# Optimization experiments

Measured on AMD Instinct MI355X. Metric: run time of the kernel, lower is better.

## Reference

```python
import jax, jax.numpy as jnp
import numpy as np

B, T, E, K, NNEG = 128, 512, 128, 4, 64


def setup_inputs() -> dict:
    key = jax.random.key(0)
    k1, k2, k3, k4 = jax.random.split(key, 4)
    base_payload = jax.random.normal(k1, (B, T, E), dtype=jnp.float32)
    mapped_ctx_payload = jax.random.normal(k2, (B, T, E, K), dtype=jnp.float32)
    seq_lens = jax.random.randint(k3, (B,), 1, T + 1, dtype=jnp.int32)
    # valid positions mask over the flattened (B*T) pool of possible negatives
    valid = (jnp.arange(T)[None, :] < seq_lens[:, None]).reshape(-1)  # [B*T]
    logits = jnp.where(valid, 0.0, -1e30)[None, :]                    # [1, B*T]
    logits = jnp.broadcast_to(logits, (B, B * T))
    # mirrors torch.multinomial(mask, n_negatives): one draw set per batch row
    sample_ids = jax.random.categorical(k4, logits, shape=(NNEG, B)).T.astype(jnp.int32)
    return {
        "base_payload": base_payload,
        "mapped_ctx_payload": mapped_ctx_payload,
        "seq_lens": seq_lens,
        "sample_ids": sample_ids,
    }


def reference(base_payload, mapped_ctx_payload, seq_lens, sample_ids):
    b, t, e = base_payload.shape
    n_steps = mapped_ctx_payload.shape[-1]
    # length mask [b, t]
    len_mask = (jnp.arange(t)[None, :] < seq_lens[:, None]).astype(base_payload.dtype)
    # zero context embeddings past each sequence's length
    trimmed_mce = mapped_ctx_payload * len_mask[:, :, None, None]  # [b, t, e, n_steps]
    # gather sampled negatives from the flattened base embedding pool
    neg_samples = base_payload.reshape(b * t, e)[sample_ids]  # [b, n_neg, e]

    step_losses = []
    for i in range(1, n_steps + 1):
        ce_i = trimmed_mce[:, : t - i, :, i - 1]   # [b, t-i, e]
        be_i = base_payload[:, i:]                  # [b, t-i, e]
        positive_pred = jnp.sum(ce_i * be_i, axis=-1)             # [b, t-i]
        neg_pred = jnp.einsum('bse,bne->bsn', ce_i, neg_samples)  # [b, t-i, n_neg]
        logits = jnp.concatenate([positive_pred[..., None], neg_pred], axis=-1)
        step_losses.append(-jax.nn.log_softmax(logits, axis=-1)[:, :, 0].mean())
    return jnp.stack(step_losses).mean()
```

## Files before the change

kernel.cpp:

```cpp
#include <hip/hip_runtime.h>
#include <math.h>

#define NB 128
#define NT 512
#define NEDIM 128
#define NNEG 64
#define SCHUNK 32
#define NBLK (NB * (NT / SCHUNK))

typedef __bf16 bf16x8 __attribute__((ext_vector_type(8)));
typedef float  f32x4  __attribute__((ext_vector_type(4)));

__launch_bounds__(256, 3)
__global__ void cpc_mfma_kernel(const float* __restrict__ base,
                                const float* __restrict__ mce,
                                const int*  __restrict__ seq_lens,
                                const int*  __restrict__ sample_ids,
                                float* __restrict__ ws)
{
    const int b    = blockIdx.y;
    const int s0   = blockIdx.x * SCHUNK;
    const int slot = b * (NT / SCHUNK) + blockIdx.x;
    const int L    = seq_lens[b];
    const float LOG65 = 4.1743873f;
    const float wgt[4] = {1.f/261632.f, 1.f/261120.f, 1.f/260608.f, 1.f/260096.f};

    if (s0 >= L) {
        if (threadIdx.x == 0) {
            float c = 0.f;
            #pragma unroll
            for (int i = 1; i <= 4; ++i) {
                int hi = min(SCHUNK, (NT - i) - s0);
                if (hi > 0) c += (float)hi * LOG65 * wgt[i - 1];
            }
            ws[slot] = c;
        }
        return;
    }

    __shared__ __bf16 Afrag[2048 * 8];
    __shared__ __bf16 Bfrag[1024 * 8];
    __shared__ float  pos_lds[128];
    __shared__ float  wsum[4];

    const int tid  = threadIdx.x;
    const int lane = tid & 63;
    const int w    = tid >> 6;
    const int q    = lane >> 4;
    const int fl   = lane & 15;

    const float4* mce4 = (const float4*)mce;

    #pragma unroll
    for (int it = 0; it < 2; ++it) {
        int g  = tid + 256 * it;
        int s  = g & 31;
        int eb = g >> 5;
        const float4* src = mce4 + (size_t)(b * NT + s0 + s) * NEDIM + eb * 8;
        float4 v[8];
        #pragma unroll
        for (int u = 0; u < 8; ++u) v[u] = src[u];
        const float* vf = (const float*)v;
        int Cs = (eb >> 2) * 8 + (s >> 2);
        int base_chunk = Cs * 64 + (eb & 3) * 16 + (s & 3) * 4;
        int x = Cs & 7;
        #pragma unroll
        for (int k = 0; k < 4; ++k) {
            int phys = (base_chunk + k) ^ x;
            bf16x8 o;
            #pragma unroll
            for (int u = 0; u < 8; ++u) o[u] = (__bf16)vf[4 * u + k];
            *(bf16x8*)(&Afrag[phys * 8]) = o;
        }
    }

    {
        int n = tid & 63;
        int r = sample_ids[b * NNEG + n];
        const float4* srcb = (const float4*)(base + (size_t)r * NEDIM);
        int eb0 = (tid >> 6) * 4;
        #pragma unroll
        for (int it = 0; it < 4; ++it) {
            int eb = eb0 + it;
            float4 v0 = srcb[eb * 2], v1 = srcb[eb * 2 + 1];
            const float* f0 = (const float*)&v0;
            const float* f1 = (const float*)&v1;
            bf16x8 o;
            #pragma unroll
            for (int u = 0; u < 4; ++u) { o[u] = (__bf16)f0[u]; o[4 + u] = (__bf16)f1[u]; }
            *(bf16x8*)(&Bfrag[(eb * 64 + n) * 8]) = o;
        }
    }
    __syncthreads();

    f32x4 acc[2][4];
    #pragma unroll
    for (int mtl = 0; mtl < 2; ++mtl)
        #pragma unroll
        for (int nt = 0; nt < 4; ++nt) acc[mtl][nt] = (f32x4){0.f, 0.f, 0.f, 0.f};

    #pragma unroll
    for (int kstep = 0; kstep < 4; ++kstep) {
        bf16x8 af[2];
        #pragma unroll
        for (int mtl = 0; mtl < 2; ++mtl) {
            int Cs = kstep * 8 + (2 * w + mtl);
            int phys = (Cs * 64 + lane) ^ (Cs & 7);
            af[mtl] = *(const bf16x8*)(&Afrag[phys * 8]);
        }
        bf16x8 bv[4];
        #pragma unroll
        for (int nt = 0; nt < 4; ++nt) {
            int cB = (kstep * 4 + q) * 64 + nt * 16 + fl;
            bv[nt] = *(const bf16x8*)(&Bfrag[cB * 8]);
        }
        #pragma unroll
        for (int mtl = 0; mtl < 2; ++mtl)
            #pragma unroll
            for (int nt = 0; nt < 4; ++nt)
                acc[mtl][nt] = __builtin_amdgcn_mfma_f32_16x16x32_bf16(
                    af[mtl], bv[nt], acc[mtl][nt], 0, 0, 0);
    }

    {
        int m    = tid >> 1;
        int eh   = tid & 1;
        int sloc = m >> 2, ip = (m & 3) + 1;
        int srow = s0 + sloc + ip; if (srow > NT - 1) srow = NT - 1;
        const float4* brow4 = (const float4*)(base + (size_t)(b * NT + srow) * NEDIM + eh * 64);
        int mt = m >> 4, flm = m & 15;
        float psum = 0.f;
        #pragma unroll
        for (int el = 0; el < 8; ++el) {
            int eb = eh * 8 + el;
            int Cs = (eb >> 2) * 8 + mt;
            int phys = (Cs * 64 + (eb & 3) * 16 + flm) ^ (Cs & 7);
            bf16x8 av = *(const bf16x8*)(&Afrag[phys * 8]);
            float4 b0 = brow4[el * 2], b1 = brow4[el * 2 + 1];
            const float* f0 = (const float*)&b0;
            const float* f1 = (const float*)&b1;
            #pragma unroll
            for (int u = 0; u < 4; ++u) {
                psum = fmaf((float)av[u],     f0[u], psum);
                psum = fmaf((float)av[4 + u], f1[u], psum);
            }
        }
        psum += __shfl_xor(psum, 1);
        if (eh == 0) pos_lds[m] = psum;
    }
    __syncthreads();

    float lossacc = 0.f;
    #pragma unroll
    for (int mtl = 0; mtl < 2; ++mtl) {
        #pragma unroll
        for (int r = 0; r < 4; ++r) {
            int m  = w * 32 + mtl * 16 + q * 4 + r;
            int sg = s0 + (m >> 2);
            int ip = (m & 3) + 1;
            float z0 = acc[mtl][0][r], z1 = acc[mtl][1][r];
            float z2 = acc[mtl][2][r], z3 = acc[mtl][3][r];
            float p  = pos_lds[m];
            float mx = fmaxf(fmaxf(z0, z1), fmaxf(z2, z3));
            mx = fmaxf(mx, __shfl_xor(mx, 1));
            mx = fmaxf(mx, __shfl_xor(mx, 2));
            mx = fmaxf(mx, __shfl_xor(mx, 4));
            mx = fmaxf(mx, __shfl_xor(mx, 8));
            mx = fmaxf(mx, p);
            float es = __expf(z0 - mx) + __expf(z1 - mx)
                     + __expf(z2 - mx) + __expf(z3 - mx);
            es += __shfl_xor(es, 1);
            es += __shfl_xor(es, 2);
            es += __shfl_xor(es, 4);
            es += __shfl_xor(es, 8);
            es += __expf(p - mx);
            float loss = __logf(es) + (mx - p);
            loss = (sg < L) ? loss : LOG65;
            bool take = (sg < NT - ip) && (fl == 0);
            lossacc += take ? wgt[ip - 1] * loss : 0.f;
        }
    }
    lossacc += __shfl_xor(lossacc, 16);
    lossacc += __shfl_xor(lossacc, 32);
    if (lane == 0) wsum[w] = lossacc;
    __syncthreads();
    if (tid == 0) ws[slot] = wsum[0] + wsum[1] + wsum[2] + wsum[3];
}

__global__ void reduce_k(const float* __restrict__ ws, float* __restrict__ out) {
    const int tid = threadIdx.x;
    float s = 0.f;
    #pragma unroll
    for (int i = 0; i < NBLK / 256; ++i) s += ws[tid + 256 * i];
    s += __shfl_xor(s, 1);
    s += __shfl_xor(s, 2);
    s += __shfl_xor(s, 4);
    s += __shfl_xor(s, 8);
    s += __shfl_xor(s, 16);
    s += __shfl_xor(s, 32);
    __shared__ float wsum[4];
    if ((tid & 63) == 0) wsum[tid >> 6] = s;
    __syncthreads();
    if (tid == 0) out[0] = wsum[0] + wsum[1] + wsum[2] + wsum[3];
}

extern "C" void kernel_launch(void* const* d_in, const int* in_sizes, int n_in,
                              void* d_out, int out_size, void* d_ws, size_t ws_size,
                              hipStream_t stream) {
    (void)in_sizes; (void)n_in; (void)out_size; (void)ws_size;
    const float* base       = (const float*)d_in[0];
    const float* mce        = (const float*)d_in[1];
    const int*   seq_lens   = (const int*)d_in[2];
    const int*   sample_ids = (const int*)d_in[3];
    float* out = (float*)d_out;
    float* ws  = (float*)d_ws;

    dim3 grid(NT / SCHUNK, NB);
    cpc_mfma_kernel<<<grid, 256, 0, stream>>>(base, mce, seq_lens, sample_ids, ws);
    reduce_k<<<1, 256, 0, stream>>>(ws, out);
}
```

Before: 224.1 us.

## Make each wave an independent 4-position tile with direct register-loaded MFMA operands

Each wavefront now handles 4 sequence positions (16 rows of 4 steps) on its own, loading the mce operand with strided scalar loads and the negative samples straight from global memory into MFMA registers. This removes the LDS staging, the swizzled fragment layout and the block-level barriers. Fully masked regions are now skipped per wave at finer granularity, and the workspace grows to one slot per wave. The cost is that the negatives are re-read per wave instead of shared across the block, and the mce reads are uncoalesced 4-byte loads with stride 16 bytes.

```diff
diff --git a/kernel.cpp b/kernel.cpp
--- a/kernel.cpp
+++ b/kernel.cpp
@@ -3,195 +3,132 @@
 
 #define NB 128
 #define NT 512
-#define NEDIM 128
+#define NE 128
 #define NNEG 64
-#define SCHUNK 32
-#define NBLK (NB * (NT / SCHUNK))
+#define NSLOT (NB * 128)
 
 typedef __bf16 bf16x8 __attribute__((ext_vector_type(8)));
 typedef float  f32x4  __attribute__((ext_vector_type(4)));
 
 __launch_bounds__(256, 3)
-__global__ void cpc_mfma_kernel(const float* __restrict__ base,
+__global__ void cpc_wave_kernel(const float* __restrict__ base,
                                 const float* __restrict__ mce,
                                 const int*  __restrict__ seq_lens,
                                 const int*  __restrict__ sample_ids,
                                 float* __restrict__ ws)
 {
-    const int b    = blockIdx.y;
-    const int s0   = blockIdx.x * SCHUNK;
-    const int slot = b * (NT / SCHUNK) + blockIdx.x;
+    const int jb   = blockIdx.x;
+    const int tid  = threadIdx.x;
+    const int w    = tid >> 6;
+    const int lane = tid & 63;
+    const int q    = lane >> 4;
+    const int fl   = lane & 15;
+    const int b    = jb >> 5;
+    const int g    = (jb & 31) * 4 + w;
+    const int s0   = g * 4;
     const int L    = seq_lens[b];
+    const int slot = b * 128 + g;
     const float LOG65 = 4.1743873f;
     const float wgt[4] = {1.f/261632.f, 1.f/261120.f, 1.f/260608.f, 1.f/260096.f};
 
     if (s0 >= L) {
-        if (threadIdx.x == 0) {
+        if (lane == 0) {
             float c = 0.f;
             #pragma unroll
             for (int i = 1; i <= 4; ++i) {
-                int hi = min(SCHUNK, (NT - i) - s0);
-                if (hi > 0) c += (float)hi * LOG65 * wgt[i - 1];
+                int cnt = min(4, max(0, (NT - i) - s0));
+                c += (float)cnt * LOG65 * wgt[i - 1];
             }
             ws[slot] = c;
         }
         return;
     }
 
-    __shared__ __bf16 Afrag[2048 * 8];
-    __shared__ __bf16 Bfrag[1024 * 8];
-    __shared__ float  pos_lds[128];
-    __shared__ float  wsum[4];
+    const int ds = fl >> 2;
+    const int ki = fl & 3;
 
-    const int tid  = threadIdx.x;
-    const int lane = tid & 63;
-    const int w    = tid >> 6;
-    const int q    = lane >> 4;
-    const int fl   = lane & 15;
+    int rid[4];
+    #pragma unroll
+    for (int nt = 0; nt < 4; ++nt)
+        rid[nt] = sample_ids[b * NNEG + nt * 16 + fl];
 
-    const float4* mce4 = (const float4*)mce;
+    const float* Arow = mce + (size_t)(b * NT + s0 + ds) * (NE * 4) + ki;
+    int sp = s0 + ds + ki + 1; if (sp > NT - 1) sp = NT - 1;
+    const float* Prow = base + (size_t)(b * NT + sp) * NE;
+
+    f32x4 acc[4];
+    #pragma unroll
+    for (int nt = 0; nt < 4; ++nt) acc[nt] = (f32x4){0.f, 0.f, 0.f, 0.f};
+    float pp = 0.f;
 
     #pragma unroll
-    for (int it = 0; it < 2; ++it) {
-        int g  = tid + 256 * it;
-        int s  = g & 31;
-        int eb = g >> 5;
-        const float4* src = mce4 + (size_t)(b * NT + s0 + s) * NEDIM + eb * 8;
-        float4 v[8];
+    for (int ks = 0; ks < 4; ++ks) {
+        const int e0 = ks * 32 + q * 8;
+        float a[8];
         #pragma unroll
-        for (int u = 0; u < 8; ++u) v[u] = src[u];
-        const float* vf = (const float*)v;
-        int Cs = (eb >> 2) * 8 + (s >> 2);
-        int base_chunk = Cs * 64 + (eb & 3) * 16 + (s & 3) * 4;
-        int x = Cs & 7;
+        for (int u = 0; u < 8; ++u) a[u] = Arow[(size_t)(e0 + u) * 4];
+        bf16x8 af;
         #pragma unroll
-        for (int k = 0; k < 4; ++k) {
-            int phys = (base_chunk + k) ^ x;
-            bf16x8 o;
-            #pragma unroll
-            for (int u = 0; u < 8; ++u) o[u] = (__bf16)vf[4 * u + k];
-            *(bf16x8*)(&Afrag[phys * 8]) = o;
+        for (int u = 0; u < 8; ++u) af[u] = (__bf16)a[u];
+        float4 p0 = *(const float4*)(Prow + e0);
+        float4 p1 = *(const float4*)(Prow + e0 + 4);
+        pp = fmaf(a[0], p0.x, pp); pp = fmaf(a[1], p0.y, pp);
+        pp = fmaf(a[2], p0.z, pp); pp = fmaf(a[3], p0.w, pp);
+        pp = fmaf(a[4], p1.x, pp); pp = fmaf(a[5], p1.y, pp);
+        pp = fmaf(a[6], p1.z, pp); pp = fmaf(a[7], p1.w, pp);
+        #pragma unroll
+        for (int nt = 0; nt < 4; ++nt) {
+            const float* Bp = base + (size_t)rid[nt] * NE + e0;
+            float4 b0 = *(const float4*)Bp;
+            float4 b1 = *(const float4*)(Bp + 4);
+            bf16x8 bv;
+            bv[0] = (__bf16)b0.x; bv[1] = (__bf16)b0.y;
+            bv[2] = (__bf16)b0.z; bv[3] = (__bf16)b0.w;
+            bv[4] = (__bf16)b1.x; bv[5] = (__bf16)b1.y;
+            bv[6] = (__bf16)b1.z; bv[7] = (__bf16)b1.w;
+            acc[nt] = __builtin_amdgcn_mfma_f32_16x16x32_bf16(af, bv, acc[nt], 0, 0, 0);
         }
     }
 
-    {
-        int n = tid & 63;
-        int r = sample_ids[b * NNEG + n];
-        const float4* srcb = (const float4*)(base + (size_t)r * NEDIM);
-        int eb0 = (tid >> 6) * 4;
-        #pragma unroll
-        for (int it = 0; it < 4; ++it) {
-            int eb = eb0 + it;
-            float4 v0 = srcb[eb * 2], v1 = srcb[eb * 2 + 1];
-            const float* f0 = (const float*)&v0;
-            const float* f1 = (const float*)&v1;
-            bf16x8 o;
-            #pragma unroll
-            for (int u = 0; u < 4; ++u) { o[u] = (__bf16)f0[u]; o[4 + u] = (__bf16)f1[u]; }
-            *(bf16x8*)(&Bfrag[(eb * 64 + n) * 8]) = o;
-        }
-    }
-    __syncthreads();
-
-    f32x4 acc[2][4];
-    #pragma unroll
-    for (int mtl = 0; mtl < 2; ++mtl)
-        #pragma unroll
-        for (int nt = 0; nt < 4; ++nt) acc[mtl][nt] = (f32x4){0.f, 0.f, 0.f, 0.f};
-
-    #pragma unroll
-    for (int kstep = 0; kstep < 4; ++kstep) {
-        bf16x8 af[2];
-        #pragma unroll
-        for (int mtl = 0; mtl < 2; ++mtl) {
-            int Cs = kstep * 8 + (2 * w + mtl);
-            int phys = (Cs * 64 + lane) ^ (Cs & 7);
-            af[mtl] = *(const bf16x8*)(&Afrag[phys * 8]);
-        }
-        bf16x8 bv[4];
-        #pragma unroll
-        for (int nt = 0; nt < 4; ++nt) {
-            int cB = (kstep * 4 + q) * 64 + nt * 16 + fl;
-            bv[nt] = *(const bf16x8*)(&Bfrag[cB * 8]);
-        }
-        #pragma unroll
-        for (int mtl = 0; mtl < 2; ++mtl)
-            #pragma unroll
-            for (int nt = 0; nt < 4; ++nt)
-                acc[mtl][nt] = __builtin_amdgcn_mfma_f32_16x16x32_bf16(
-                    af[mtl], bv[nt], acc[mtl][nt], 0, 0, 0);
-    }
-
-    {
-        int m    = tid >> 1;
-        int eh   = tid & 1;
-        int sloc = m >> 2, ip = (m & 3) + 1;
-        int srow = s0 + sloc + ip; if (srow > NT - 1) srow = NT - 1;
-        const float4* brow4 = (const float4*)(base + (size_t)(b * NT + srow) * NEDIM + eh * 64);
-        int mt = m >> 4, flm = m & 15;
-        float psum = 0.f;
-        #pragma unroll
-        for (int el = 0; el < 8; ++el) {
-            int eb = eh * 8 + el;
-            int Cs = (eb >> 2) * 8 + mt;
-            int phys = (Cs * 64 + (eb & 3) * 16 + flm) ^ (Cs & 7);
-            bf16x8 av = *(const bf16x8*)(&Afrag[phys * 8]);
-            float4 b0 = brow4[el * 2], b1 = brow4[el * 2 + 1];
-            const float* f0 = (const float*)&b0;
-            const float* f1 = (const float*)&b1;
-            #pragma unroll
-            for (int u = 0; u < 4; ++u) {
-                psum = fmaf((float)av[u],     f0[u], psum);
-                psum = fmaf((float)av[4 + u], f1[u], psum);
-            }
-        }
-        psum += __shfl_xor(psum, 1);
-        if (eh == 0) pos_lds[m] = psum;
-    }
-    __syncthreads();
+    pp += __shfl_xor(pp, 16);
+    pp += __shfl_xor(pp, 32);
 
     float lossacc = 0.f;
     #pragma unroll
-    for (int mtl = 0; mtl < 2; ++mtl) {
-        #pragma unroll
-        for (int r = 0; r < 4; ++r) {
-            int m  = w * 32 + mtl * 16 + q * 4 + r;
-            int sg = s0 + (m >> 2);
-            int ip = (m & 3) + 1;
-            float z0 = acc[mtl][0][r], z1 = acc[mtl][1][r];
-            float z2 = acc[mtl][2][r], z3 = acc[mtl][3][r];
-            float p  = pos_lds[m];
-            float mx = fmaxf(fmaxf(z0, z1), fmaxf(z2, z3));
-            mx = fmaxf(mx, __shfl_xor(mx, 1));
-            mx = fmaxf(mx, __shfl_xor(mx, 2));
-            mx = fmaxf(mx, __shfl_xor(mx, 4));
-            mx = fmaxf(mx, __shfl_xor(mx, 8));
-            mx = fmaxf(mx, p);
-            float es = __expf(z0 - mx) + __expf(z1 - mx)
-                     + __expf(z2 - mx) + __expf(z3 - mx);
-            es += __shfl_xor(es, 1);
-            es += __shfl_xor(es, 2);
-            es += __shfl_xor(es, 4);
-            es += __shfl_xor(es, 8);
-            es += __expf(p - mx);
-            float loss = __logf(es) + (mx - p);
-            loss = (sg < L) ? loss : LOG65;
-            bool take = (sg < NT - ip) && (fl == 0);
-            lossacc += take ? wgt[ip - 1] * loss : 0.f;
-        }
+    for (int r = 0; r < 4; ++r) {
+        int row = q * 4 + r;
+        int s   = s0 + (row >> 2);
+        int ip  = (row & 3) + 1;
+        float p = __shfl(pp, row);
+        float z0 = acc[0][r], z1 = acc[1][r], z2 = acc[2][r], z3 = acc[3][r];
+        float mx = fmaxf(fmaxf(z0, z1), fmaxf(z2, z3));
+        mx = fmaxf(mx, __shfl_xor(mx, 1));
+        mx = fmaxf(mx, __shfl_xor(mx, 2));
+        mx = fmaxf(mx, __shfl_xor(mx, 4));
+        mx = fmaxf(mx, __shfl_xor(mx, 8));
+        mx = fmaxf(mx, p);
+        float es = __expf(z0 - mx) + __expf(z1 - mx)
+                 + __expf(z2 - mx) + __expf(z3 - mx);
+        es += __shfl_xor(es, 1);
+        es += __shfl_xor(es, 2);
+        es += __shfl_xor(es, 4);
+        es += __shfl_xor(es, 8);
+        es += __expf(p - mx);
+        float loss = __logf(es) + (mx - p);
+        loss = (s < L) ? loss : LOG65;
+        bool take = (s < NT - ip) && (fl == 0);
+        lossacc += take ? wgt[ip - 1] * loss : 0.f;
     }
     lossacc += __shfl_xor(lossacc, 16);
     lossacc += __shfl_xor(lossacc, 32);
-    if (lane == 0) wsum[w] = lossacc;
-    __syncthreads();
-    if (tid == 0) ws[slot] = wsum[0] + wsum[1] + wsum[2] + wsum[3];
+    if (lane == 0) ws[slot] = lossacc;
 }
 
 __global__ void reduce_k(const float* __restrict__ ws, float* __restrict__ out) {
     const int tid = threadIdx.x;
     float s = 0.f;
     #pragma unroll
-    for (int i = 0; i < NBLK / 256; ++i) s += ws[tid + 256 * i];
+    for (int i = 0; i < NSLOT / 256; ++i) s += ws[tid + 256 * i];
     s += __shfl_xor(s, 1);
     s += __shfl_xor(s, 2);
     s += __shfl_xor(s, 4);
@@ -215,7 +152,6 @@
     float* out = (float*)d_out;
     float* ws  = (float*)d_ws;
 
-    dim3 grid(NT / SCHUNK, NB);
-    cpc_mfma_kernel<<<grid, 256, 0, stream>>>(base, mce, seq_lens, sample_ids, ws);
+    cpc_wave_kernel<<<dim3(NB * 32), 256, 0, stream>>>(base, mce, seq_lens, sample_ids, ws);
     reduce_k<<<1, 256, 0, stream>>>(ws, out);
 }
```

New measurement: 257.3 us. 1.15x slower.
